# Performance work log

Measured on AMD Instinct MI355X. Metric: run time of the kernel, lower is better.

The kernel has to match this reference:

```python
import jax, jax.numpy as jnp
import numpy as np

HEADS, MAX_SEQ, N_STATE = 8, 2048, 512
DEPTH = N_STATE // HEADS
B, S = 2, 2048
EPS = 1e-5


def setup_inputs() -> dict:
    key = jax.random.key(0)
    ks = jax.random.split(key, 8)
    sd = lambda f: 1.0 / np.sqrt(f)
    causal = jnp.tril(jnp.ones((S, S), dtype=bool))
    mask = jnp.where(causal, 0.0, -1e9).astype(jnp.float32)[None, None]
    return {
        "x": jax.random.normal(ks[0], (B, S, N_STATE), jnp.float32),
        "mask": mask,
        "W_qkv": jax.random.normal(ks[1], (N_STATE, 3 * N_STATE), jnp.float32) * sd(N_STATE),
        "b_qkv": jnp.zeros((3 * N_STATE,), jnp.float32),
        "W_proj": jax.random.normal(ks[2], (N_STATE, N_STATE), jnp.float32) * sd(N_STATE),
        "b_proj": jnp.zeros((N_STATE,), jnp.float32),
        "E": jax.random.normal(ks[3], (HEADS, MAX_SEQ, DEPTH), jnp.float32) * sd(DEPTH),
        "g1": jnp.ones((N_STATE,), jnp.float32),
        "be1": jnp.zeros((N_STATE,), jnp.float32),
        "g2": jnp.ones((N_STATE,), jnp.float32),
        "be2": jnp.zeros((N_STATE,), jnp.float32),
        "W_fc1": jax.random.normal(ks[4], (N_STATE, 4 * N_STATE), jnp.float32) * sd(N_STATE),
        "b_fc1": jnp.zeros((4 * N_STATE,), jnp.float32),
        "W_fc2": jax.random.normal(ks[5], (4 * N_STATE, N_STATE), jnp.float32) * sd(4 * N_STATE),
        "b_fc2": jnp.zeros((N_STATE,), jnp.float32),
    }


def _layernorm(x, g, b):
    mu = jnp.mean(x, axis=-1, keepdims=True)
    var = jnp.mean(jnp.square(x - mu), axis=-1, keepdims=True)
    return (x - mu) * jax.lax.rsqrt(var + EPS) * g + b


def _relative_skew(rel):
    # rel: [B, H, S, S] = q @ E_slice^T ; skew trick -> relative positions
    b, h, s, _ = rel.shape
    rel = jnp.pad(rel, ((0, 0), (0, 0), (0, 0), (1, 0)))  # [B,H,S,S+1]
    rel = rel.reshape(b, h, s + 1, s)
    return rel[:, :, 1:, :]  # [B,H,S,S]


def reference(x, mask, W_qkv, b_qkv, W_proj, b_proj, E, g1, be1, g2, be2,
              W_fc1, b_fc1, W_fc2, b_fc2):
    b, s, _ = x.shape
    a = _layernorm(x, g1, be1)
    qkv = a @ W_qkv + b_qkv  # [B,S,3N]
    q, k, v = jnp.split(qkv, 3, axis=-1)
    split = lambda t: t.reshape(b, s, HEADS, DEPTH).transpose(0, 2, 1, 3)  # [B,H,S,D]
    q, k, v = split(q), split(k), split(v)
    present = jnp.stack([k, v], axis=1)  # [B,2,H,S,D]

    w = jnp.einsum("bhqd,bhkd->bhqk", q, k)
    E_s = E[:, MAX_SEq if False else MAX_SEQ - s:, :]  # [H,S,D]
    rel = jnp.einsum("bhqd,hld->bhql", q, E_s)
    w = (w + _relative_skew(rel)) * (1.0 / np.sqrt(DEPTH))
    w = w + mask
    w = jax.nn.softmax(w, axis=-1)
    att = jnp.einsum("bhqk,bhkd->bhqd", w, v)
    att = att.transpose(0, 2, 1, 3).reshape(b, s, N_STATE)
    att = att @ W_proj + b_proj

    x = x + att
    m = _layernorm(x, g2, be2)
    m = jax.nn.gelu(m @ W_fc1 + b_fc1) @ W_fc2 + b_fc2
    x = x + m
    return (x, present)
```

## Files before the change

### kernel.cpp

```cpp
#include <hip/hip_runtime.h>
#include <stdint.h>

#define DEV __device__ __forceinline__

typedef __attribute__((ext_vector_type(8))) short bf16x8;
typedef __attribute__((ext_vector_type(4))) float f32x4;

DEV ushort f2bf(float f) {
  union { float f; uint32_t u; } c; c.f = f;
  return (ushort)((c.u + 0x7FFFu + ((c.u >> 16) & 1)) >> 16);
}
DEV bf16x8 ld8(const ushort* p) { return *reinterpret_cast<const bf16x8*>(p); }

DEV void gload16(const void* g, void* l) {
  __builtin_amdgcn_global_load_lds(
      (const __attribute__((address_space(1))) uint32_t*)g,
      (__attribute__((address_space(3))) uint32_t*)l, 16, 0, 0);
}

__global__ __launch_bounds__(256) void k_transpose_bf(const float* __restrict__ in,
                                                      ushort* __restrict__ out,
                                                      int R, int C) {
  __shared__ float t[32][33];
  int tx = threadIdx.x & 31, ty = threadIdx.x >> 5;
  int c0 = blockIdx.x * 32, r0 = blockIdx.y * 32;
#pragma unroll
  for (int k = 0; k < 4; ++k)
    t[ty + 8 * k][tx] = in[(size_t)(r0 + ty + 8 * k) * C + c0 + tx];
  __syncthreads();
#pragma unroll
  for (int k = 0; k < 4; ++k)
    out[(size_t)(c0 + ty + 8 * k) * R + r0 + tx] = f2bf(t[tx][ty + 8 * k]);
}

__global__ __launch_bounds__(256) void k_cvt_bf(const float* __restrict__ in,
                                                ushort* __restrict__ out, int n4) {
  int i = blockIdx.x * 256 + threadIdx.x;
  if (i >= n4) return;
  float4 v = reinterpret_cast<const float4*>(in)[i];
  ushort4 o; o.x = f2bf(v.x); o.y = f2bf(v.y); o.z = f2bf(v.z); o.w = f2bf(v.w);
  reinterpret_cast<ushort4*>(out)[i] = o;
}

__global__ __launch_bounds__(256) void k_ln(const float* __restrict__ x,
                                            const float* __restrict__ g,
                                            const float* __restrict__ be,
                                            ushort* __restrict__ out) {
  int w = threadIdx.x >> 6, lane = threadIdx.x & 63;
  int row = blockIdx.x * 4 + w;
  const float* xr = x + (size_t)row * 512 + lane * 8;
  float4 a = *reinterpret_cast<const float4*>(xr);
  float4 b = *reinterpret_cast<const float4*>(xr + 4);
  float xs[8] = {a.x, a.y, a.z, a.w, b.x, b.y, b.z, b.w};
  float s = 0.f, q = 0.f;
#pragma unroll
  for (int i = 0; i < 8; ++i) { s += xs[i]; q += xs[i] * xs[i]; }
#pragma unroll
  for (int off = 32; off; off >>= 1) { s += __shfl_xor(s, off); q += __shfl_xor(q, off); }
  float mu = s * (1.f / 512.f);
  float var = q * (1.f / 512.f) - mu * mu;
  float inv = rsqrtf(var + 1e-5f);
  const float* gp = g + lane * 8;
  const float* bp = be + lane * 8;
  ushort o[8];
#pragma unroll
  for (int i = 0; i < 8; ++i) o[i] = f2bf((xs[i] - mu) * inv * gp[i] + bp[i]);
  *reinterpret_cast<uint4*>(out + (size_t)row * 512 + lane * 8) = *reinterpret_cast<uint4*>(o);
}

template <int EPI, int BN>
__global__ __launch_bounds__(256) void k_gemm(
    const ushort* __restrict__ A, const ushort* __restrict__ Bt,
    int M, int N, int K,
    const float* __restrict__ bias, const float* __restrict__ res,
    float* __restrict__ outf, ushort* __restrict__ outb,
    float* __restrict__ present, ushort* __restrict__ qbf,
    ushort* __restrict__ kbf, ushort* __restrict__ vtbf) {
  constexpr int NF = BN / 32;
  __shared__ ushort As[128][64];
  __shared__ ushort Bs[BN][64];
  const int tid = threadIdx.x, lane = tid & 63, w = tid >> 6;
  const int g = lane >> 4, l16 = lane & 15;
  const int m0 = blockIdx.y * 128, n0 = blockIdx.x * BN;
  const int wm = (w >> 1) * 64, wn = (w & 1) * (BN / 2);
  f32x4 acc[4][NF];
#pragma unroll
  for (int i = 0; i < 4; ++i)
#pragma unroll
    for (int j = 0; j < NF; ++j) acc[i][j] = (f32x4){0.f, 0.f, 0.f, 0.f};

  const int lrow_off = (lane << 4);
  for (int k0 = 0; k0 < K; k0 += 64) {
#pragma unroll
    for (int sw = 0; sw < 4; ++sw) {
      int offb = sw * 4096 + w * 1024;
      int loff = offb + lrow_off;
      int row = loff >> 7, colb = loff & 127;
      gload16((const char*)A + (((size_t)(m0 + row) * K + k0) << 1) + colb,
              (char*)As + offb);
    }
#pragma unroll
    for (int sw = 0; sw < BN / 32; ++sw) {
      int offb = sw * 4096 + w * 1024;
      int loff = offb + lrow_off;
      int row = loff >> 7, colb = loff & 127;
      gload16((const char*)Bt + (((size_t)(n0 + row) * K + k0) << 1) + colb,
              (char*)Bs + offb);
    }
    __syncthreads();
#pragma unroll
    for (int kk = 0; kk < 2; ++kk) {
      bf16x8 af[4], bfr[NF];
#pragma unroll
      for (int f = 0; f < 4; ++f)
        af[f] = *reinterpret_cast<const bf16x8*>(&As[wm + f * 16 + l16][kk * 32 + g * 8]);
#pragma unroll
      for (int f = 0; f < NF; ++f)
        bfr[f] = *reinterpret_cast<const bf16x8*>(&Bs[wn + f * 16 + l16][kk * 32 + g * 8]);
#pragma unroll
      for (int i = 0; i < 4; ++i)
#pragma unroll
        for (int j = 0; j < NF; ++j)
          acc[i][j] = __builtin_amdgcn_mfma_f32_16x16x32_bf16(af[i], bfr[j], acc[i][j], 0, 0, 0);
    }
    __syncthreads();
  }

#pragma unroll
  for (int i = 0; i < 4; ++i)
#pragma unroll
    for (int j = 0; j < NF; ++j)
#pragma unroll
      for (int r = 0; r < 4; ++r) {
        int row = m0 + wm + i * 16 + g * 4 + r;
        int col = n0 + wn + j * 16 + l16;
        float v = acc[i][j][r] + bias[col];
        if constexpr (EPI == 0) {
          int third = col >> 9, hh = (col >> 6) & 7, d = col & 63;
          int bb = row >> 11, sq = row & 2047;
          if (third == 0) {
            qbf[((((size_t)bb * 8 + hh) * 2048) + sq) * 64 + d] = f2bf(v);
          } else {
            present[((((size_t)bb * 2 + (third - 1)) * 8 + hh) * 2048 + sq) * 64 + d] = v;
            if (third == 1)
              kbf[((((size_t)bb * 8 + hh) * 2048) + sq) * 64 + d] = f2bf(v);
            else
              vtbf[(((size_t)bb * 8 + hh) * 64 + d) * 2048 + sq] = f2bf(v);
          }
        } else if constexpr (EPI == 1) {
          size_t idx = (size_t)row * N + col;
          outf[idx] = v + res[idx];
        } else {
          float u = 0.7978845608f * (v + 0.044715f * v * v * v);
          float e = __expf(2.f * u);
          float th = 1.f - 2.f / (e + 1.f);
          outb[(size_t)row * N + col] = f2bf(0.5f * v * (1.f + th));
        }
      }
}

__global__ __launch_bounds__(128, 4) void k_attn(
    const ushort* __restrict__ qbf, const ushort* __restrict__ kbf,
    const ushort* __restrict__ vtbf, const ushort* __restrict__ Ebf,
    ushort* __restrict__ attb) {
  constexpr int S = 2048;
  constexpr int REG = 5376 + 2432;
  __shared__ alignas(16) char pool[2 * REG];
  const int tid = threadIdx.x, lane = tid & 63, ks = tid >> 6;
  const int g = lane >> 4, l16 = lane & 15;
  const int bid = blockIdx.x;
  const int h = bid & 7, rest = bid >> 3;
  const int b = rest & 1, t = 127 - (rest >> 1);
  const int bh = b * 8 + h;
  float(*Rs)[84] = (float(*)[84])(pool + ks * REG);
  ushort(*Ps)[76] = (ushort(*)[76])(pool + ks * REG + 5376);
  float* Mrg = (float*)(pool + REG);

  const ushort* qp = qbf + (size_t)bh * S * 64;
  const ushort* kp = kbf + (size_t)bh * S * 64;
  const ushort* vp = vtbf + (size_t)bh * 64 * S;
  const ushort* ep = Ebf + (size_t)h * S * 64;

  const int i0 = t * 16;
  bf16x8 qf[2];
  qf[0] = ld8(qp + (size_t)(i0 + l16) * 64 + g * 8);
  qf[1] = ld8(qp + (size_t)(i0 + l16) * 64 + 32 + g * 8);
  f32x4 o[4];
#pragma unroll
  for (int fv = 0; fv < 4; ++fv) o[fv] = (f32x4){0.f, 0.f, 0.f, 0.f};
  float mrun[4], lrun[4];
#pragma unroll
  for (int r = 0; r < 4; ++r) { mrun[r] = -1e30f; lrun[r] = 0.f; }
  const int nkt = (t + 4) >> 2;

  for (int kt = ks; kt < nkt; kt += 2) {
    const int j0 = kt * 64;
    f32x4 sacc[4];
#pragma unroll
    for (int fn = 0; fn < 4; ++fn) sacc[fn] = (f32x4){0.f, 0.f, 0.f, 0.f};
#pragma unroll
    for (int kk = 0; kk < 2; ++kk)
#pragma unroll
      for (int fn = 0; fn < 4; ++fn) {
        bf16x8 kf = ld8(kp + (size_t)(j0 + fn * 16 + l16) * 64 + kk * 32 + g * 8);
        sacc[fn] = __builtin_amdgcn_mfma_f32_16x16x32_bf16(qf[kk], kf, sacc[fn], 0, 0, 0);
      }
    const int tb = S - 16 - i0 + j0;
    f32x4 racc[5];
#pragma unroll
    for (int fc = 0; fc < 5; ++fc) racc[fc] = (f32x4){0.f, 0.f, 0.f, 0.f};
#pragma unroll
    for (int kk = 0; kk < 2; ++kk)
#pragma unroll
      for (int fc = 0; fc < 5; ++fc) {
        int l = tb + fc * 16 + l16; if (l > S - 1) l = S - 1;
        bf16x8 ef = ld8(ep + (size_t)l * 64 + kk * 32 + g * 8);
        racc[fc] = __builtin_amdgcn_mfma_f32_16x16x32_bf16(qf[kk], ef, racc[fc], 0, 0, 0);
      }
#pragma unroll
    for (int fc = 0; fc < 5; ++fc)
#pragma unroll
      for (int r = 0; r < 4; ++r)
        Rs[g * 4 + r][fc * 16 + l16] = racc[fc][r];

    float Sv[4][4], mtile[4];
#pragma unroll
    for (int r = 0; r < 4; ++r) mtile[r] = -1e30f;
#pragma unroll
    for (int fn = 0; fn < 4; ++fn)
#pragma unroll
      for (int r = 0; r < 4; ++r) {
        int dr = g * 4 + r, dj = fn * 16 + l16;
        float sv = (sacc[fn][r] + Rs[dr][15 - dr + dj]) * 0.125f;
        if (j0 + dj > i0 + dr) sv = -1e30f;
        Sv[fn][r] = sv;
        mtile[r] = fmaxf(mtile[r], sv);
      }
#pragma unroll
    for (int off = 1; off < 16; off <<= 1)
#pragma unroll
      for (int r = 0; r < 4; ++r) mtile[r] = fmaxf(mtile[r], __shfl_xor(mtile[r], off));
    float corr[4], psum[4];
#pragma unroll
    for (int r = 0; r < 4; ++r) {
      float mn = fmaxf(mrun[r], mtile[r]);
      corr[r] = __expf(mrun[r] - mn);
      mrun[r] = mn;
      psum[r] = 0.f;
    }
#pragma unroll
    for (int fn = 0; fn < 4; ++fn)
#pragma unroll
      for (int r = 0; r < 4; ++r) {
        float pv = __expf(Sv[fn][r] - mrun[r]);
        psum[r] += pv;
        Ps[g * 4 + r][fn * 16 + l16] = f2bf(pv);
      }
#pragma unroll
    for (int off = 1; off < 16; off <<= 1)
#pragma unroll
      for (int r = 0; r < 4; ++r) psum[r] += __shfl_xor(psum[r], off);
#pragma unroll
    for (int r = 0; r < 4; ++r) lrun[r] = lrun[r] * corr[r] + psum[r];
#pragma unroll
    for (int fv = 0; fv < 4; ++fv)
#pragma unroll
      for (int r = 0; r < 4; ++r) o[fv][r] *= corr[r];

#pragma unroll
    for (int kk = 0; kk < 2; ++kk) {
      bf16x8 pf = ld8(&Ps[l16][kk * 32 + g * 8]);
#pragma unroll
      for (int fv = 0; fv < 4; ++fv) {
        bf16x8 vf = ld8(vp + (size_t)(fv * 16 + l16) * S + j0 + kk * 32 + g * 8);
        o[fv] = __builtin_amdgcn_mfma_f32_16x16x32_bf16(pf, vf, o[fv], 0, 0, 0);
      }
    }
  }

  if (ks == 1) {
    float* mb = Mrg + lane * 24;
#pragma unroll
    for (int fv = 0; fv < 4; ++fv)
#pragma unroll
      for (int r = 0; r < 4; ++r) mb[fv * 4 + r] = o[fv][r];
#pragma unroll
    for (int r = 0; r < 4; ++r) { mb[16 + r] = mrun[r]; mb[20 + r] = lrun[r]; }
  }
  __syncthreads();
  if (ks == 0) {
    const float* mb = Mrg + lane * 24;
#pragma unroll
    for (int r = 0; r < 4; ++r) {
      float m1 = mb[16 + r];
      float mm = fmaxf(mrun[r], m1);
      float e0 = __expf(mrun[r] - mm), e1 = __expf(m1 - mm);
      float lc = lrun[r] * e0 + mb[20 + r] * e1;
      float inv = 1.f / lc;
#pragma unroll
      for (int fv = 0; fv < 4; ++fv) {
        float oc = o[fv][r] * e0 + mb[fv * 4 + r] * e1;
        attb[(size_t)(b * S + i0 + g * 4 + r) * 512 + h * 64 + fv * 16 + l16] =
            f2bf(oc * inv);
      }
    }
  }
}

extern "C" void kernel_launch(void* const* d_in, const int* in_sizes, int n_in,
                              void* d_out, int out_size, void* d_ws, size_t ws_size,
                              hipStream_t stream) {
  const float* x = (const float*)d_in[0];
  const float* W_qkv = (const float*)d_in[2];
  const float* b_qkv = (const float*)d_in[3];
  const float* W_proj = (const float*)d_in[4];
  const float* b_proj = (const float*)d_in[5];
  const float* E = (const float*)d_in[6];
  const float* g1 = (const float*)d_in[7];
  const float* be1 = (const float*)d_in[8];
  const float* g2 = (const float*)d_in[9];
  const float* be2 = (const float*)d_in[10];
  const float* W_fc1 = (const float*)d_in[11];
  const float* b_fc1 = (const float*)d_in[12];
  const float* W_fc2 = (const float*)d_in[13];
  const float* b_fc2 = (const float*)d_in[14];

  float* x_out = (float*)d_out;
  float* present = x_out + 2097152;

  char* ws = (char*)d_ws;
  ushort* a_bf   = (ushort*)(ws + 0);
  ushort* m_bf   = (ushort*)(ws + 4194304);
  ushort* q_bf   = (ushort*)(ws + 8388608);
  ushort* att_bf = (ushort*)(ws + 12582912);
  ushort* h_bf   = (ushort*)(ws + 16777216);
  ushort* k_bf   = (ushort*)(ws + 16777216);
  ushort* vt_bf  = (ushort*)(ws + 20971520);
  float*  x2     = (float*)(ws + 33554432);
  ushort* Wqkv_t = (ushort*)(ws + 41943040);
  ushort* Wproj_t= (ushort*)(ws + 43515904);
  ushort* Wfc1_t = (ushort*)(ws + 44040192);
  ushort* Wfc2_t = (ushort*)(ws + 46137344);
  ushort* E_bf   = (ushort*)(ws + 48234496);

  k_transpose_bf<<<dim3(48, 16), 256, 0, stream>>>(W_qkv, Wqkv_t, 512, 1536);
  k_transpose_bf<<<dim3(16, 16), 256, 0, stream>>>(W_proj, Wproj_t, 512, 512);
  k_transpose_bf<<<dim3(64, 16), 256, 0, stream>>>(W_fc1, Wfc1_t, 512, 2048);
  k_transpose_bf<<<dim3(16, 64), 256, 0, stream>>>(W_fc2, Wfc2_t, 2048, 512);
  k_cvt_bf<<<1024, 256, 0, stream>>>(E, E_bf, 262144);
  k_ln<<<1024, 256, 0, stream>>>(x, g1, be1, a_bf);
  k_gemm<0, 128><<<dim3(12, 32), 256, 0, stream>>>(a_bf, Wqkv_t, 4096, 1536, 512,
                                                   b_qkv, nullptr, nullptr, nullptr,
                                                   present, q_bf, k_bf, vt_bf);
  k_attn<<<2048, 128, 0, stream>>>(q_bf, k_bf, vt_bf, E_bf, att_bf);
  k_gemm<1, 64><<<dim3(8, 32), 256, 0, stream>>>(att_bf, Wproj_t, 4096, 512, 512,
                                                 b_proj, x, x2, nullptr, nullptr, nullptr,
                                                 nullptr, nullptr);
  k_ln<<<1024, 256, 0, stream>>>(x2, g2, be2, m_bf);
  k_gemm<2, 128><<<dim3(16, 32), 256, 0, stream>>>(m_bf, Wfc1_t, 4096, 2048, 512,
                                                   b_fc1, nullptr, nullptr, h_bf, nullptr,
                                                   nullptr, nullptr, nullptr);
  k_gemm<1, 64><<<dim3(8, 32), 256, 0, stream>>>(h_bf, Wfc2_t, 4096, 512, 2048,
                                                 b_fc2, x2, x_out, nullptr, nullptr, nullptr,
                                                 nullptr, nullptr);
}
```

Baseline: 331.5 us.

## Double-buffer GEMM tiles and do relative skew with lane shuffles in attention

The GEMM kernel now double-buffers its A/B LDS tiles, issuing the next K-tile's global-to-LDS loads before computing on the current one. This is meant to overlap memory with MFMA work, but the doubled shared memory may reduce occupancy. In the attention kernel, all K, E and V fragments for a tile are loaded into registers up front, and the relative-position skew uses cross-lane shuffles instead of an LDS round trip. This frees LDS, but the extra live registers led to lowering launch bounds occupancy from 4 to 2.

```diff
diff --git a/kernel.cpp b/kernel.cpp
--- a/kernel.cpp
+++ b/kernel.cpp
@@ -77,8 +77,8 @@
     float* __restrict__ present, ushort* __restrict__ qbf,
     ushort* __restrict__ kbf, ushort* __restrict__ vtbf) {
   constexpr int NF = BN / 32;
-  __shared__ ushort As[128][64];
-  __shared__ ushort Bs[BN][64];
+  __shared__ ushort As[2][128][64];
+  __shared__ ushort Bs[2][BN][64];
   const int tid = threadIdx.x, lane = tid & 63, w = tid >> 6;
   const int g = lane >> 4, l16 = lane & 15;
   const int m0 = blockIdx.y * 128, n0 = blockIdx.x * BN;
@@ -90,14 +90,14 @@
     for (int j = 0; j < NF; ++j) acc[i][j] = (f32x4){0.f, 0.f, 0.f, 0.f};
 
   const int lrow_off = (lane << 4);
-  for (int k0 = 0; k0 < K; k0 += 64) {
+  auto stage = [&](int buf, int k0) {
 #pragma unroll
     for (int sw = 0; sw < 4; ++sw) {
       int offb = sw * 4096 + w * 1024;
       int loff = offb + lrow_off;
       int row = loff >> 7, colb = loff & 127;
       gload16((const char*)A + (((size_t)(m0 + row) * K + k0) << 1) + colb,
-              (char*)As + offb);
+              (char*)(&As[buf][0][0]) + offb);
     }
 #pragma unroll
     for (int sw = 0; sw < BN / 32; ++sw) {
@@ -105,18 +105,25 @@
       int loff = offb + lrow_off;
       int row = loff >> 7, colb = loff & 127;
       gload16((const char*)Bt + (((size_t)(n0 + row) * K + k0) << 1) + colb,
-              (char*)Bs + offb);
-    }
-    __syncthreads();
+              (char*)(&Bs[buf][0][0]) + offb);
+    }
+  };
+
+  const int nt = K >> 6;
+  stage(0, 0);
+  __syncthreads();
+  for (int t = 0; t < nt; ++t) {
+    const int cur = t & 1;
+    if (t + 1 < nt) stage(cur ^ 1, (t + 1) << 6);
 #pragma unroll
     for (int kk = 0; kk < 2; ++kk) {
       bf16x8 af[4], bfr[NF];
 #pragma unroll
       for (int f = 0; f < 4; ++f)
-        af[f] = *reinterpret_cast<const bf16x8*>(&As[wm + f * 16 + l16][kk * 32 + g * 8]);
+        af[f] = *reinterpret_cast<const bf16x8*>(&As[cur][wm + f * 16 + l16][kk * 32 + g * 8]);
 #pragma unroll
       for (int f = 0; f < NF; ++f)
-        bfr[f] = *reinterpret_cast<const bf16x8*>(&Bs[wn + f * 16 + l16][kk * 32 + g * 8]);
+        bfr[f] = *reinterpret_cast<const bf16x8*>(&Bs[cur][wn + f * 16 + l16][kk * 32 + g * 8]);
 #pragma unroll
       for (int i = 0; i < 4; ++i)
 #pragma unroll
@@ -159,22 +166,19 @@
       }
 }
 
-__global__ __launch_bounds__(128, 4) void k_attn(
+__global__ __launch_bounds__(128, 2) void k_attn(
     const ushort* __restrict__ qbf, const ushort* __restrict__ kbf,
     const ushort* __restrict__ vtbf, const ushort* __restrict__ Ebf,
     ushort* __restrict__ attb) {
   constexpr int S = 2048;
-  constexpr int REG = 5376 + 2432;
-  __shared__ alignas(16) char pool[2 * REG];
+  __shared__ ushort Ps[2][16][76];
+  __shared__ float Mrg[64][24];
   const int tid = threadIdx.x, lane = tid & 63, ks = tid >> 6;
   const int g = lane >> 4, l16 = lane & 15;
   const int bid = blockIdx.x;
   const int h = bid & 7, rest = bid >> 3;
   const int b = rest & 1, t = 127 - (rest >> 1);
   const int bh = b * 8 + h;
-  float(*Rs)[84] = (float(*)[84])(pool + ks * REG);
-  ushort(*Ps)[76] = (ushort(*)[76])(pool + ks * REG + 5376);
-  float* Mrg = (float*)(pool + REG);
 
   const ushort* qp = qbf + (size_t)bh * S * 64;
   const ushort* kp = kbf + (size_t)bh * S * 64;
@@ -195,47 +199,66 @@
 
   for (int kt = ks; kt < nkt; kt += 2) {
     const int j0 = kt * 64;
+    const int tb = S - 16 - i0 + j0;
+    bf16x8 kf[8], ef[10], vf[8];
+#pragma unroll
+    for (int fn = 0; fn < 4; ++fn) {
+      const ushort* kr = kp + (size_t)(j0 + fn * 16 + l16) * 64 + g * 8;
+      kf[fn] = ld8(kr);
+      kf[4 + fn] = ld8(kr + 32);
+    }
+#pragma unroll
+    for (int fc = 0; fc < 5; ++fc) {
+      int l = tb + fc * 16 + l16; if (l > S - 1) l = S - 1;
+      const ushort* er = ep + (size_t)l * 64 + g * 8;
+      ef[fc] = ld8(er);
+      ef[5 + fc] = ld8(er + 32);
+    }
+#pragma unroll
+    for (int fv = 0; fv < 4; ++fv) {
+      const ushort* vr = vp + (size_t)(fv * 16 + l16) * S + j0 + g * 8;
+      vf[fv] = ld8(vr);
+      vf[4 + fv] = ld8(vr + 32);
+    }
+
     f32x4 sacc[4];
 #pragma unroll
     for (int fn = 0; fn < 4; ++fn) sacc[fn] = (f32x4){0.f, 0.f, 0.f, 0.f};
 #pragma unroll
     for (int kk = 0; kk < 2; ++kk)
 #pragma unroll
+      for (int fn = 0; fn < 4; ++fn)
+        sacc[fn] = __builtin_amdgcn_mfma_f32_16x16x32_bf16(qf[kk], kf[kk * 4 + fn], sacc[fn], 0, 0, 0);
+
+    f32x4 racc[5];
+#pragma unroll
+    for (int fc = 0; fc < 5; ++fc) racc[fc] = (f32x4){0.f, 0.f, 0.f, 0.f};
+#pragma unroll
+    for (int kk = 0; kk < 2; ++kk)
+#pragma unroll
+      for (int fc = 0; fc < 5; ++fc)
+        racc[fc] = __builtin_amdgcn_mfma_f32_16x16x32_bf16(qf[kk], ef[kk * 5 + fc], racc[fc], 0, 0, 0);
+
+    float Sv[4][4], mtile[4];
+#pragma unroll
+    for (int r = 0; r < 4; ++r) mtile[r] = -1e30f;
+#pragma unroll
+    for (int r = 0; r < 4; ++r) {
+      const int dr = g * 4 + r;
+      const int src = (lane & 48) | ((l16 + 15 - dr) & 15);
+      const bool hi = (l16 > dr);
+#pragma unroll
       for (int fn = 0; fn < 4; ++fn) {
-        bf16x8 kf = ld8(kp + (size_t)(j0 + fn * 16 + l16) * 64 + kk * 32 + g * 8);
-        sacc[fn] = __builtin_amdgcn_mfma_f32_16x16x32_bf16(qf[kk], kf, sacc[fn], 0, 0, 0);
-      }
-    const int tb = S - 16 - i0 + j0;
-    f32x4 racc[5];
-#pragma unroll
-    for (int fc = 0; fc < 5; ++fc) racc[fc] = (f32x4){0.f, 0.f, 0.f, 0.f};
-#pragma unroll
-    for (int kk = 0; kk < 2; ++kk)
-#pragma unroll
-      for (int fc = 0; fc < 5; ++fc) {
-        int l = tb + fc * 16 + l16; if (l > S - 1) l = S - 1;
-        bf16x8 ef = ld8(ep + (size_t)l * 64 + kk * 32 + g * 8);
-        racc[fc] = __builtin_amdgcn_mfma_f32_16x16x32_bf16(qf[kk], ef, racc[fc], 0, 0, 0);
-      }
-#pragma unroll
-    for (int fc = 0; fc < 5; ++fc)
-#pragma unroll
-      for (int r = 0; r < 4; ++r)
-        Rs[g * 4 + r][fc * 16 + l16] = racc[fc][r];
-
-    float Sv[4][4], mtile[4];
-#pragma unroll
-    for (int r = 0; r < 4; ++r) mtile[r] = -1e30f;
-#pragma unroll
-    for (int fn = 0; fn < 4; ++fn)
-#pragma unroll
-      for (int r = 0; r < 4; ++r) {
-        int dr = g * 4 + r, dj = fn * 16 + l16;
-        float sv = (sacc[fn][r] + Rs[dr][15 - dr + dj]) * 0.125f;
+        float lo_v = __shfl(racc[fn][r], src);
+        float hi_v = __shfl(racc[fn + 1][r], src);
+        float rel = hi ? hi_v : lo_v;
+        float sv = (sacc[fn][r] + rel) * 0.125f;
+        int dj = fn * 16 + l16;
         if (j0 + dj > i0 + dr) sv = -1e30f;
         Sv[fn][r] = sv;
         mtile[r] = fmaxf(mtile[r], sv);
       }
+    }
 #pragma unroll
     for (int off = 1; off < 16; off <<= 1)
 #pragma unroll
@@ -254,7 +277,7 @@
       for (int r = 0; r < 4; ++r) {
         float pv = __expf(Sv[fn][r] - mrun[r]);
         psum[r] += pv;
-        Ps[g * 4 + r][fn * 16 + l16] = f2bf(pv);
+        Ps[ks][g * 4 + r][fn * 16 + l16] = f2bf(pv);
       }
 #pragma unroll
     for (int off = 1; off < 16; off <<= 1)
@@ -269,17 +292,15 @@
 
 #pragma unroll
     for (int kk = 0; kk < 2; ++kk) {
-      bf16x8 pf = ld8(&Ps[l16][kk * 32 + g * 8]);
-#pragma unroll
-      for (int fv = 0; fv < 4; ++fv) {
-        bf16x8 vf = ld8(vp + (size_t)(fv * 16 + l16) * S + j0 + kk * 32 + g * 8);
-        o[fv] = __builtin_amdgcn_mfma_f32_16x16x32_bf16(pf, vf, o[fv], 0, 0, 0);
-      }
+      bf16x8 pf = ld8(&Ps[ks][l16][kk * 32 + g * 8]);
+#pragma unroll
+      for (int fv = 0; fv < 4; ++fv)
+        o[fv] = __builtin_amdgcn_mfma_f32_16x16x32_bf16(pf, vf[kk * 4 + fv], o[fv], 0, 0, 0);
     }
   }
 
   if (ks == 1) {
-    float* mb = Mrg + lane * 24;
+    float* mb = &Mrg[lane][0];
 #pragma unroll
     for (int fv = 0; fv < 4; ++fv)
 #pragma unroll
@@ -289,7 +310,7 @@
   }
   __syncthreads();
   if (ks == 0) {
-    const float* mb = Mrg + lane * 24;
+    const float* mb = &Mrg[lane][0];
 #pragma unroll
     for (int r = 0; r < 4; ++r) {
       float m1 = mb[16 + r];
```

New measurement: 322.4 us. 2.7% less time.
